# Kernel tuning notes

Measured on AMD Instinct MI355X. Metric: run time of the kernel, lower is better.

Reference implementation:

```python
import jax, jax.numpy as jnp
import numpy as np

B, S, D, H = 2, 2048, 1024, 16
HD = D // H
LOCAL_WINDOW = 32
GLOBAL_TOKENS = 16
BLOCK_SIZE = 64
SPARSITY = 0.75


def _structured_mask(seq_len):
    """local_global | block_sparse pattern, vectorized numpy (deterministic)."""
    i = np.arange(seq_len)[:, None]
    j = np.arange(seq_len)[None, :]
    half = LOCAL_WINDOW // 2
    local = np.abs(i - j) <= half  # mask[i, i-16 : i+17]
    glob = (i < GLOBAL_TOKENS) | (j < GLOBAL_TOKENS)
    stride = max(1, seq_len // 64)
    strided = ((i % stride) == 0) & ((j % stride) == 0)
    lg = local | glob | strided
    # block sparse: random blocks kept with prob 1-SPARSITY, diagonal always kept
    nb = (seq_len + BLOCK_SIZE - 1) // BLOCK_SIZE
    rng = np.random.default_rng(0)
    block_mask = rng.random((nb, nb)) > SPARSITY
    np.fill_diagonal(block_mask, True)
    bs = np.kron(block_mask, np.ones((BLOCK_SIZE, BLOCK_SIZE), dtype=bool))[:seq_len, :seq_len]
    return lg | bs


def setup_inputs() -> dict:
    key = jax.random.key(0)
    ks = jax.random.split(key, 12)
    std = 1.0 / np.sqrt(D)
    inp = {
        'query': jax.random.normal(ks[0], (B, S, D), jnp.float32),
        'key': jax.random.normal(ks[1], (B, S, D), jnp.float32),
        'value': jax.random.normal(ks[2], (B, S, D), jnp.float32),
        'Wq': jax.random.normal(ks[3], (D, D), jnp.float32) * std,
        'bq': jnp.zeros((D,), jnp.float32),
        'Wk': jax.random.normal(ks[4], (D, D), jnp.float32) * std,
        'bk': jnp.zeros((D,), jnp.float32),
        'Wv': jax.random.normal(ks[5], (D, D), jnp.float32) * std,
        'bv': jnp.zeros((D,), jnp.float32),
        'Wo': jax.random.normal(ks[6], (D, D), jnp.float32) * std,
        'bo': jnp.zeros((D,), jnp.float32),
        'sparse_mask': jnp.asarray(_structured_mask(S)),
    }
    return inp


def reference(query, key, value, Wq, bq, Wk, bk, Wv, bv, Wo, bo, sparse_mask):
    scale = HD ** -0.5
    # projections -> [B, H, S, HD]
    q = (query @ Wq + bq).reshape(B, S, H, HD).transpose(0, 2, 1, 3)
    k = (key @ Wk + bk).reshape(B, S, H, HD).transpose(0, 2, 1, 3)
    v = (value @ Wv + bv).reshape(B, S, H, HD).transpose(0, 2, 1, 3)
    # dense scores then structured sparse mask (matches original math)
    scores = jnp.einsum('bhqd,bhkd->bhqk', q, k) * scale
    scores = jnp.where(sparse_mask[None, None], scores, -jnp.inf)
    attn = jax.nn.softmax(scores, axis=-1)  # every row has >=1 active entry (global cols)
    out = jnp.einsum('bhqk,bhkd->bhqd', attn, v)
    out = out.transpose(0, 2, 1, 3).reshape(B, S, D)
    out = out @ Wo + bo
    return out, attn
```

## Files before the change

### kernel.cpp

```cpp
#include <hip/hip_runtime.h>
#include <hip/hip_bf16.h>
#include <hip/hip_fp16.h>

using u16 = unsigned short;
using u32 = unsigned int;
using u64 = unsigned long long;

typedef __attribute__((ext_vector_type(8))) short short8;
typedef __attribute__((ext_vector_type(8))) _Float16 half8;
typedef __attribute__((ext_vector_type(4))) _Float16 half4;
typedef __attribute__((ext_vector_type(4))) float f32x4;
typedef __attribute__((ext_vector_type(2))) u32 u32x2;

#define DEVI static __device__ __forceinline__

DEVI float bfu2f(u16 u) { return __builtin_bit_cast(float, (u32)u << 16); }
DEVI u16 f2bfu(float f) { return __builtin_bit_cast(u16, __float2bfloat16(f)); }
DEVI u16 f2hu(float f) { return __builtin_bit_cast(u16, (_Float16)f); }

DEVI f32x4 mfma_f16_(half8 a, half8 b, f32x4 c) {
  return __builtin_amdgcn_mfma_f32_16x16x32_f16(a, b, c, 0, 0, 0);
}
DEVI f32x4 mfma16_f16_(half4 a, half4 b, f32x4 c) {
  return __builtin_amdgcn_mfma_f32_16x16x16f16(a, b, c, 0, 0, 0);
}

#define GLD_LDS16(src, dst) \
  __builtin_amdgcn_global_load_lds((const __attribute__((address_space(1))) void*)(src), \
                                   (__attribute__((address_space(3))) void*)(dst), 16, 0, 0)

#define BAR() __builtin_amdgcn_s_barrier()
#define VMCNT(n) asm volatile("s_waitcnt vmcnt(" #n ")" ::: "memory")

static constexpr int Bsz = 2, S = 2048, D = 1024, H = 16, HD = 64;
static constexpr int MROWS = Bsz * S;
static constexpr size_t OUT_ELEMS = (size_t)Bsz * S * D;
static constexpr float C_EXP2 = 0.18033688f;
static constexpr size_t OFF_WT  = 0;
static constexpr size_t OFF_Q   = 0x800000;
static constexpr size_t OFF_K   = 0x1000000;
static constexpr size_t OFF_V   = 0x1800000;
static constexpr size_t OFF_VT  = 0x2000000;
static constexpr size_t OFF_O   = 0x2800000;
static constexpr size_t OFF_MB  = 0x3000000;
static constexpr size_t OFF_FLG = 0x3080000;

__global__ __launch_bounds__(256) void detect_dtype(
    const u16* __restrict__ q, int* __restrict__ flag)
{
  __shared__ u32 red[256];
  const int tid = threadIdx.x;
  u32 mx = 0;
  for (int i = tid; i < 32768; i += 256) {
    u32 e = (q[2 * i] >> 7) & 0xFF;
    mx = mx > e ? mx : e;
  }
  red[tid] = mx;
  __syncthreads();
  if (tid == 0) {
    u32 m = 0;
    for (int i = 0; i < 256; ++i) m = m > red[i] ? m : red[i];
    flag[0] = (m >= 0x90) ? 1 : 0;
  }
}

__global__ __launch_bounds__(256) void prep_w(
    const void* __restrict__ Wq, const void* __restrict__ Wk,
    const void* __restrict__ Wv, const void* __restrict__ Wo,
    u16* __restrict__ WT, const int* __restrict__ flag)
{
  __shared__ _Float16 t[64][80];
  const int z = blockIdx.z;
  const void* src = z == 0 ? Wq : z == 1 ? Wk : z == 2 ? Wv : Wo;
  u16* dst = WT + (size_t)z * 1024 * 1024;
  const int bx = blockIdx.x, by = blockIdx.y;
  const int tid = threadIdx.x;
  const int r = tid >> 2, ch = tid & 3;
  const int fl = *flag;
  if (fl) {
    const float* s = (const float*)src + (size_t)(by * 64 + r) * 1024 + bx * 64 + ch * 16;
    #pragma unroll
    for (int v = 0; v < 4; ++v) {
      float4 f = ((const float4*)s)[v];
      t[r][ch * 16 + v * 4 + 0] = (_Float16)f.x;
      t[r][ch * 16 + v * 4 + 1] = (_Float16)f.y;
      t[r][ch * 16 + v * 4 + 2] = (_Float16)f.z;
      t[r][ch * 16 + v * 4 + 3] = (_Float16)f.w;
    }
  } else {
    const u16* s = (const u16*)src + (size_t)(by * 64 + r) * 1024 + bx * 64 + ch * 16;
    uint4 a0 = ((const uint4*)s)[0], a1 = ((const uint4*)s)[1];
    u32 wds[8] = {a0.x, a0.y, a0.z, a0.w, a1.x, a1.y, a1.z, a1.w};
    #pragma unroll
    for (int j = 0; j < 8; ++j) {
      t[r][ch * 16 + 2 * j]     = (_Float16)bfu2f((u16)(wds[j] & 0xFFFF));
      t[r][ch * 16 + 2 * j + 1] = (_Float16)bfu2f((u16)(wds[j] >> 16));
    }
  }
  __syncthreads();
  half8 o0, o1;
  #pragma unroll
  for (int i = 0; i < 8; ++i) { o0[i] = t[ch * 16 + i][r]; o1[i] = t[ch * 16 + 8 + i][r]; }
  u16* d = dst + (size_t)(bx * 64 + r) * 1024 + by * 64 + ch * 16;
  *reinterpret_cast<half8*>(d) = o0;
  *reinterpret_cast<half8*>(d + 8) = o1;
}

__global__ __launch_bounds__(256) void mask_bits_kernel(
    const void* __restrict__ mask, u64* __restrict__ mbits)
{
  const u32 w0 = *(const u32*)mask;
  int mode;
  if (w0 == 0x01010101u) mode = 0;
  else if ((w0 & 0xFFFFu) && (w0 >> 16)) mode = 1;
  else mode = 2;
  const int row = blockIdx.x;
  const int w = threadIdx.x >> 6, l = threadIdx.x & 63;
  for (int i = 0; i < 8; ++i) {
    int jw = w * 8 + i;
    size_t idx = (size_t)row * S + jw * 64 + l;
    bool m;
    if (mode == 0)      m = ((const unsigned char*)mask)[idx] != 0;
    else if (mode == 1) m = ((const u16*)mask)[idx] != 0;
    else                m = ((const u32*)mask)[idx] != 0;
    u64 bal = __ballot(m);
    if (l == 0) mbits[(size_t)row * 32 + jw] = bal;
  }
}

template<int A_DYN, int OUT_DYN>
DEVI void gemm_body(const void* __restrict__ A, const _Float16* __restrict__ Bt,
                    const void* __restrict__ bias, void* __restrict__ C,
                    int fl, int tM, int tN, int N, int K,
                    _Float16* As, _Float16* Bs)
{
  const int tid = threadIdx.x;
  const int w = tid >> 6, l = tid & 63;
  const int wr = w >> 1, wc = w & 1;
  const int lg = l >> 4, lc = l & 15;
  const int rr = l >> 3;
  const int gsw = (l & 7) ^ rr;
  const int rsw = lc & 7;
  const int arow = tid >> 2, ach = tid & 3;

  f32x4 acc[2][4] = {};

  for (int k0 = 0; k0 < K; k0 += 64) {
    if (A_DYN) {
      half8 h0, h1;
      if (fl) {
        const float* ap = (const float*)A + (size_t)(tM + arow) * K + k0 + ach * 16;
        float4 f0 = ((const float4*)ap)[0], f1 = ((const float4*)ap)[1];
        float4 f2 = ((const float4*)ap)[2], f3 = ((const float4*)ap)[3];
        h0[0] = (_Float16)f0.x; h0[1] = (_Float16)f0.y;
        h0[2] = (_Float16)f0.z; h0[3] = (_Float16)f0.w;
        h0[4] = (_Float16)f1.x; h0[5] = (_Float16)f1.y;
        h0[6] = (_Float16)f1.z; h0[7] = (_Float16)f1.w;
        h1[0] = (_Float16)f2.x; h1[1] = (_Float16)f2.y;
        h1[2] = (_Float16)f2.z; h1[3] = (_Float16)f2.w;
        h1[4] = (_Float16)f3.x; h1[5] = (_Float16)f3.y;
        h1[6] = (_Float16)f3.z; h1[7] = (_Float16)f3.w;
      } else {
        const u16* ap = (const u16*)A + (size_t)(tM + arow) * K + k0 + ach * 16;
        uint4 a0 = ((const uint4*)ap)[0], a1 = ((const uint4*)ap)[1];
        u32 wd[8] = {a0.x, a0.y, a0.z, a0.w, a1.x, a1.y, a1.z, a1.w};
        #pragma unroll
        for (int j = 0; j < 4; ++j) {
          h0[2 * j]     = (_Float16)bfu2f((u16)(wd[j] & 0xFFFF));
          h0[2 * j + 1] = (_Float16)bfu2f((u16)(wd[j] >> 16));
          h1[2 * j]     = (_Float16)bfu2f((u16)(wd[4 + j] & 0xFFFF));
          h1[2 * j + 1] = (_Float16)bfu2f((u16)(wd[4 + j] >> 16));
        }
      }
      const int c0 = (2 * ach) ^ (arow & 7), c1 = (2 * ach + 1) ^ (arow & 7);
      *reinterpret_cast<half8*>(&As[arow * 64 + c0 * 8]) = h0;
      *reinterpret_cast<half8*>(&As[arow * 64 + c1 * 8]) = h1;
    } else {
      #pragma unroll
      for (int s = 0; s < 2; ++s)
        GLD_LDS16((const _Float16*)A + (size_t)(tM + w * 16 + s * 8 + rr) * K + k0 + gsw * 8,
                  &As[(w * 16 + s * 8) * 64]);
    }
    #pragma unroll
    for (int s = 0; s < 4; ++s)
      GLD_LDS16(Bt + (size_t)(tN + w * 32 + s * 8 + rr) * K + k0 + gsw * 8,
                &Bs[(w * 32 + s * 8) * 64]);
    __syncthreads();
    half8 a[2][2], b[4][2];
    #pragma unroll
    for (int m = 0; m < 2; ++m)
      #pragma unroll
      for (int kk = 0; kk < 2; ++kk)
        a[m][kk] = *reinterpret_cast<const half8*>(
            &As[(wr * 32 + m * 16 + lc) * 64 + ((kk * 4 + lg) ^ rsw) * 8]);
    #pragma unroll
    for (int n = 0; n < 4; ++n)
      #pragma unroll
      for (int kk = 0; kk < 2; ++kk)
        b[n][kk] = *reinterpret_cast<const half8*>(
            &Bs[(wc * 64 + n * 16 + lc) * 64 + ((kk * 4 + lg) ^ rsw) * 8]);
    #pragma unroll
    for (int m = 0; m < 2; ++m)
      #pragma unroll
      for (int n = 0; n < 4; ++n) {
        acc[m][n] = mfma_f16_(a[m][0], b[n][0], acc[m][n]);
        acc[m][n] = mfma_f16_(a[m][1], b[n][1], acc[m][n]);
      }
    __syncthreads();
  }

  float bf[4];
  #pragma unroll
  for (int n = 0; n < 4; ++n) {
    int col = tN + wc * 64 + n * 16 + lc;
    bf[n] = fl ? ((const float*)bias)[col] : bfu2f(((const u16*)bias)[col]);
  }
  #pragma unroll
  for (int m = 0; m < 2; ++m) {
    int row = tM + wr * 32 + m * 16 + lg * 4;
    #pragma unroll
    for (int n = 0; n < 4; ++n) {
      int col = tN + wc * 64 + n * 16 + lc;
      #pragma unroll
      for (int r = 0; r < 4; ++r) {
        float v = acc[m][n][r] + bf[n];
        size_t off = (size_t)(row + r) * N + col;
        if (OUT_DYN) {
          if (fl) ((float*)C)[off] = v;
          else    ((u16*)C)[off] = f2bfu(v);
        } else {
          ((u16*)C)[off] = f2hu(v);
        }
      }
    }
  }
}

__global__ __launch_bounds__(256) void gemm_qkv(
    const void* __restrict__ Aq, const void* __restrict__ Ak,
    const void* __restrict__ Av, const u16* __restrict__ WT,
    const void* __restrict__ bq, const void* __restrict__ bk,
    const void* __restrict__ bv,
    u16* __restrict__ Qb, u16* __restrict__ Kb, u16* __restrict__ Vb,
    const int* __restrict__ flag)
{
  __shared__ _Float16 As[64 * 64];
  __shared__ _Float16 Bs[128 * 64];
  const int z = blockIdx.z;
  const void* A = z == 0 ? Aq : z == 1 ? Ak : Av;
  const _Float16* Bt = (const _Float16*)(WT + (size_t)z * 1048576);
  const void* bias = z == 0 ? bq : z == 1 ? bk : bv;
  void* C = z == 0 ? Qb : z == 1 ? Kb : Vb;
  gemm_body<1, 0>(A, Bt, bias, C, *flag,
                  blockIdx.x * 64, blockIdx.y * 128, D, D, As, Bs);
}

__global__ __launch_bounds__(256) void gemm_o(
    const _Float16* __restrict__ A, const u16* __restrict__ WoT,
    const void* __restrict__ bias, void* __restrict__ C,
    const int* __restrict__ flag)
{
  __shared__ _Float16 As[64 * 64];
  __shared__ _Float16 Bs[128 * 64];
  gemm_body<0, 1>(A, (const _Float16*)WoT, bias, C, *flag,
                  blockIdx.x * 64, blockIdx.y * 128, D, D, As, Bs);
}

__global__ __launch_bounds__(256) void transpose_v(
    const _Float16* __restrict__ V, _Float16* __restrict__ vT)
{
  __shared__ _Float16 t[64][80];
  const int sb = blockIdx.x, bh = blockIdx.y;
  const int b = bh >> 4, h = bh & 15;
  const int tid = threadIdx.x;
  #pragma unroll
  for (int rep = 0; rep < 2; ++rep) {
    int idx = rep * 256 + tid;
    int sl = idx >> 3, ch = idx & 7;
    *reinterpret_cast<uint4*>(&t[sl][ch * 8]) =
      *reinterpret_cast<const uint4*>(V + (size_t)(b * S + sb * 64 + sl) * D + h * HD + ch * 8);
  }
  __syncthreads();
  #pragma unroll
  for (int rep = 0; rep < 2; ++rep) {
    int idx = rep * 256 + tid;
    int hd = idx >> 3, ch = idx & 7;
    half8 ov;
    #pragma unroll
    for (int i = 0; i < 8; ++i) ov[i] = t[ch * 8 + i][hd];
    *reinterpret_cast<half8*>(vT + ((size_t)bh * HD + hd) * S + sb * 64 + ch * 8) = ov;
  }
}

__global__ __launch_bounds__(256) void attn_kernel(
    const _Float16* __restrict__ Q, const _Float16* __restrict__ Kp,
    const _Float16* __restrict__ vT, const u64* __restrict__ mbits,
    _Float16* __restrict__ O, void* __restrict__ dOut,
    const int* __restrict__ flag)
{
  __shared__ _Float16 Ks[2][4096];
  __shared__ _Float16 Vs[2][4096];

  const int tid = threadIdx.x, w = tid >> 6, l = tid & 63;
  const int lg = l >> 4, lc = l & 15;
  const int flat = blockIdx.y * 32 + blockIdx.x;
  const int nf = (flat & 7) * 128 + (flat >> 3);
  const int rb = nf & 31, bh = nf >> 5;
  const int b = bh >> 4, h = bh & 15;
  const int wg = w ^ (rb & 1);
  const int wrow = rb * 64 + wg * 16;
  const int fl = *flag;

  half8 aq[2];
  {
    const _Float16* qp = Q + (size_t)(b * S + wrow + lc) * D + h * HD;
    aq[0] = *reinterpret_cast<const half8*>(qp + lg * 8);
    aq[1] = *reinterpret_cast<const half8*>(qp + 32 + lg * 8);
  }
  const _Float16* kbase = Kp + (size_t)(b * S) * D + h * HD;
  const _Float16* vbase = vT + (size_t)bh * HD * S;
  const u64* mrow = mbits + (size_t)(wrow + lc) * 32;

  const int rr = w * 8 + (l >> 3);
  const int gsw = (l & 7) ^ (rr & 7);

  #define STAGE_K(buf, jb) do { \
    const _Float16* s0_ = kbase + (size_t)((jb) * 64 + rr) * D + gsw * 8; \
    GLD_LDS16(s0_, &Ks[buf][w * 512]); \
    GLD_LDS16(s0_ + (size_t)32 * D, &Ks[buf][2048 + w * 512]); \
  } while (0)
  #define STAGE_V(buf, jb) do { \
    const _Float16* s0_ = vbase + (size_t)rr * S + (jb) * 64 + gsw * 8; \
    GLD_LDS16(s0_, &Vs[buf][w * 512]); \
    GLD_LDS16(s0_ + (size_t)32 * S, &Vs[buf][2048 + w * 512]); \
  } while (0)

  const int sw = lc & 7;

  float rs = 0.f;
  f32x4 accO[4] = {};

  STAGE_K(0, 0);
  STAGE_V(0, 0);
  u64 mb = mrow[0];

  #pragma unroll 1
  for (int jb = 0; jb < 32; ++jb) {
    const int buf = jb & 1;
    BAR();
    if (jb < 31) {
      STAGE_K(buf ^ 1, jb + 1);
      STAGE_V(buf ^ 1, jb + 1);
      VMCNT(5);
    } else {
      VMCNT(1);
    }
    BAR();
    const u64 mb_next = (jb < 31) ? mrow[jb + 1] : 0ull;
    const _Float16* kt = Ks[buf];
    const _Float16* vt = Vs[buf];
    #pragma unroll
    for (int c = 0; c < 4; ++c) {
      const u32 bits = (u32)(mb >> (c * 16 + lg * 4)) & 0xFu;
      if (__any(bits != 0)) {
        const int r = c * 16 + lc;
        half8 ka = *reinterpret_cast<const half8*>(&kt[r * 64 + ((lg ^ sw) * 8)]);
        half8 kb = *reinterpret_cast<const half8*>(&kt[r * 64 + (((lg + 4) ^ sw) * 8)]);
        f32x4 sc = {};
        sc = mfma_f16_(ka, aq[0], sc);
        sc = mfma_f16_(kb, aq[1], sc);
        half4 pa;
        #pragma unroll
        for (int r2 = 0; r2 < 4; ++r2) {
          float p = ((bits >> r2) & 1) ? exp2f(sc[r2] * C_EXP2) : 0.f;
          rs += p;
          pa[r2] = (_Float16)p;
        }
        #pragma unroll
        for (int d = 0; d < 4; ++d) {
          const int rd = d * 16 + lc;
          const int ch = (2 * c + (lg >> 1)) ^ sw;
          half4 vv = *reinterpret_cast<const half4*>(&vt[rd * 64 + ch * 8 + (lg & 1) * 4]);
          accO[d] = mfma16_f16_(pa, vv, accO[d]);
        }
      }
    }
    mb = mb_next;
  }

  rs += __shfl_xor(rs, 16);
  rs += __shfl_xor(rs, 32);
  const float inv = 1.f / rs;
  const float lg2i = -__log2f(rs);

  float invr[4];
  #pragma unroll
  for (int r = 0; r < 4; ++r) invr[r] = __shfl(inv, lg * 4 + r);

  {
    _Float16* op = O + (size_t)(b * S + wrow + lg * 4) * D + h * HD;
    #pragma unroll
    for (int d = 0; d < 4; ++d)
      #pragma unroll
      for (int r = 0; r < 4; ++r)
        op[(size_t)r * D + d * 16 + lc] = (_Float16)(accO[d][r] * invr[r]);
  }

  STAGE_K(0, 0);
  mb = mrow[0];

  if (fl) {
    float* ar = (float*)dOut + OUT_ELEMS + (size_t)bh * S * S + (size_t)(wrow + lc) * S;
    #pragma unroll 1
    for (int jb = 0; jb < 32; ++jb) {
      const int buf = jb & 1;
      BAR();
      if (jb < 31) { STAGE_K(buf ^ 1, jb + 1); VMCNT(7); }
      else VMCNT(5);
      BAR();
      const u64 mb_next = (jb < 31) ? mrow[jb + 1] : 0ull;
      const _Float16* kt = Ks[buf];
      #pragma unroll
      for (int c = 0; c < 4; ++c) {
        const u32 bits = (u32)(mb >> (c * 16 + lg * 4)) & 0xFu;
        f32x4* dst = (f32x4*)(ar + jb * 64 + c * 16 + lg * 4);
        if (__any(bits != 0)) {
          const int r = c * 16 + lc;
          half8 ka = *reinterpret_cast<const half8*>(&kt[r * 64 + ((lg ^ sw) * 8)]);
          half8 kb = *reinterpret_cast<const half8*>(&kt[r * 64 + (((lg + 4) ^ sw) * 8)]);
          f32x4 sc = {};
          sc = mfma_f16_(ka, aq[0], sc);
          sc = mfma_f16_(kb, aq[1], sc);
          f32x4 pv;
          #pragma unroll
          for (int r2 = 0; r2 < 4; ++r2)
            pv[r2] = ((bits >> r2) & 1) ? exp2f(__builtin_fmaf(sc[r2], C_EXP2, lg2i)) : 0.f;
          *dst = pv;
        } else {
          f32x4 z = {};
          *dst = z;
        }
      }
      mb = mb_next;
    }
  } else {
    u16* ar = (u16*)dOut + OUT_ELEMS + (size_t)bh * S * S + (size_t)(wrow + lc) * S;
    #pragma unroll 1
    for (int jb = 0; jb < 32; ++jb) {
      const int buf = jb & 1;
      BAR();
      if (jb < 31) { STAGE_K(buf ^ 1, jb + 1); VMCNT(7); }
      else VMCNT(5);
      BAR();
      const u64 mb_next = (jb < 31) ? mrow[jb + 1] : 0ull;
      const _Float16* kt = Ks[buf];
      #pragma unroll
      for (int c = 0; c < 4; ++c) {
        const u32 bits = (u32)(mb >> (c * 16 + lg * 4)) & 0xFu;
        u32x2* dst = (u32x2*)(ar + jb * 64 + c * 16 + lg * 4);
        if (__any(bits != 0)) {
          const int r = c * 16 + lc;
          half8 ka = *reinterpret_cast<const half8*>(&kt[r * 64 + ((lg ^ sw) * 8)]);
          half8 kb = *reinterpret_cast<const half8*>(&kt[r * 64 + (((lg + 4) ^ sw) * 8)]);
          f32x4 sc = {};
          sc = mfma_f16_(ka, aq[0], sc);
          sc = mfma_f16_(kb, aq[1], sc);
          float p0 = ((bits >> 0) & 1) ? exp2f(__builtin_fmaf(sc[0], C_EXP2, lg2i)) : 0.f;
          float p1 = ((bits >> 1) & 1) ? exp2f(__builtin_fmaf(sc[1], C_EXP2, lg2i)) : 0.f;
          float p2 = ((bits >> 2) & 1) ? exp2f(__builtin_fmaf(sc[2], C_EXP2, lg2i)) : 0.f;
          float p3 = ((bits >> 3) & 1) ? exp2f(__builtin_fmaf(sc[3], C_EXP2, lg2i)) : 0.f;
          u32x2 pk;
          pk[0] = (u32)f2bfu(p0) | ((u32)f2bfu(p1) << 16);
          pk[1] = (u32)f2bfu(p2) | ((u32)f2bfu(p3) << 16);
          *dst = pk;
        } else {
          u32x2 z = {0, 0};
          *dst = z;
        }
      }
      mb = mb_next;
    }
  }
  #undef STAGE_K
  #undef STAGE_V
}

extern "C" void kernel_launch(void* const* d_in, const int* in_sizes, int n_in,
                              void* d_out, int out_size, void* d_ws, size_t ws_size,
                              hipStream_t stream) {
  const void* query = d_in[0];
  const void* key_  = d_in[1];
  const void* value = d_in[2];
  const void* Wq = d_in[3];  const void* bq = d_in[4];
  const void* Wk = d_in[5];  const void* bk = d_in[6];
  const void* Wv = d_in[7];  const void* bv = d_in[8];
  const void* Wo = d_in[9];  const void* bo = d_in[10];
  const void* mask = d_in[11];

  char* ws = (char*)d_ws;
  u16* WT   = (u16*)(ws + OFF_WT);
  u16* Qb   = (u16*)(ws + OFF_Q);
  u16* Kb   = (u16*)(ws + OFF_K);
  u16* Vb   = (u16*)(ws + OFF_V);
  u16* vTb  = (u16*)(ws + OFF_VT);
  u16* Ob   = (u16*)(ws + OFF_O);
  u64* mbits = (u64*)(ws + OFF_MB);
  int* flag  = (int*)(ws + OFF_FLG);

  u16* WoT = WT + 3145728;

  detect_dtype<<<1, 256, 0, stream>>>((const u16*)query, flag);
  prep_w<<<dim3(16, 16, 4), 256, 0, stream>>>(Wq, Wk, Wv, Wo, WT, flag);
  mask_bits_kernel<<<dim3(S), 256, 0, stream>>>(mask, mbits);

  gemm_qkv<<<dim3(MROWS / 64, D / 128, 3), 256, 0, stream>>>(
      query, key_, value, WT, bq, bk, bv, Qb, Kb, Vb, flag);

  transpose_v<<<dim3(32, 32), 256, 0, stream>>>((const _Float16*)Vb, (_Float16*)vTb);
  attn_kernel<<<dim3(32, 32), 256, 0, stream>>>(
      (const _Float16*)Qb, (const _Float16*)Kb, (const _Float16*)vTb,
      mbits, (_Float16*)Ob, d_out, flag);
  gemm_o<<<dim3(MROWS / 64, D / 128), 256, 0, stream>>>(
      (const _Float16*)Ob, WoT, bo, d_out, flag);
}
```

Before: 326.3 us.

## Split attention into output pass and separate column-halved probability-write kernel

The fused attention kernel is split in two. The first pass computes the output and stores per-row log-sum values to workspace. A second kernel, launched after the output projection, recomputes the scores and writes the dense attention-probability matrix. That second kernel uses twice as many blocks, each covering half the key columns, to spread the large store across more workgroups. The cost is recomputing QK^T and an extra launch, in exchange for more parallelism on the store-bound probability write and shorter per-block work.

```diff
diff --git a/kernel.cpp b/kernel.cpp
--- a/kernel.cpp
+++ b/kernel.cpp
@@ -44,6 +44,7 @@
 static constexpr size_t OFF_O   = 0x2800000;
 static constexpr size_t OFF_MB  = 0x3000000;
 static constexpr size_t OFF_FLG = 0x3080000;
+static constexpr size_t OFF_LGI = 0x3081000;
 
 __global__ __launch_bounds__(256) void detect_dtype(
     const u16* __restrict__ q, int* __restrict__ flag)
@@ -292,11 +293,10 @@
   }
 }
 
-__global__ __launch_bounds__(256) void attn_kernel(
+__global__ __launch_bounds__(256) void attn1_kernel(
     const _Float16* __restrict__ Q, const _Float16* __restrict__ Kp,
     const _Float16* __restrict__ vT, const u64* __restrict__ mbits,
-    _Float16* __restrict__ O, void* __restrict__ dOut,
-    const int* __restrict__ flag)
+    _Float16* __restrict__ O, float* __restrict__ lgi)
 {
   __shared__ _Float16 Ks[2][4096];
   __shared__ _Float16 Vs[2][4096];
@@ -309,7 +309,6 @@
   const int b = bh >> 4, h = bh & 15;
   const int wg = w ^ (rb & 1);
   const int wrow = rb * 64 + wg * 16;
-  const int fl = *flag;
 
   half8 aq[2];
   {
@@ -387,11 +386,12 @@
     }
     mb = mb_next;
   }
+  #undef STAGE_K
+  #undef STAGE_V
 
   rs += __shfl_xor(rs, 16);
   rs += __shfl_xor(rs, 32);
   const float inv = 1.f / rs;
-  const float lg2i = -__log2f(rs);
 
   float invr[4];
   #pragma unroll
@@ -406,19 +406,63 @@
         op[(size_t)r * D + d * 16 + lc] = (_Float16)(accO[d][r] * invr[r]);
   }
 
-  STAGE_K(0, 0);
-  mb = mrow[0];
+  if (l < 16) lgi[(size_t)bh * S + wrow + l] = -__log2f(rs);
+}
+
+__global__ __launch_bounds__(256) void attn2_kernel(
+    const _Float16* __restrict__ Q, const _Float16* __restrict__ Kp,
+    const u64* __restrict__ mbits, const float* __restrict__ lgi,
+    void* __restrict__ dOut, const int* __restrict__ flag)
+{
+  __shared__ _Float16 Ks[2][4096];
+
+  const int tid = threadIdx.x, w = tid >> 6, l = tid & 63;
+  const int lg = l >> 4, lc = l & 15;
+  const int flat = blockIdx.x;
+  const int nf = (flat & 7) * 256 + (flat >> 3);
+  const int bh = nf >> 6;
+  const int rem = nf & 63;
+  const int rb = rem >> 1, half = rem & 1;
+  const int b = bh >> 4, h = bh & 15;
+  const int wg = w ^ (rb & 1);
+  const int wrow = rb * 64 + wg * 16;
+  const int fl = *flag;
+
+  half8 aq[2];
+  {
+    const _Float16* qp = Q + (size_t)(b * S + wrow + lc) * D + h * HD;
+    aq[0] = *reinterpret_cast<const half8*>(qp + lg * 8);
+    aq[1] = *reinterpret_cast<const half8*>(qp + 32 + lg * 8);
+  }
+  const _Float16* kbase = Kp + (size_t)(b * S) * D + h * HD;
+  const u64* mrow = mbits + (size_t)(wrow + lc) * 32;
+  const float lg2i = lgi[(size_t)bh * S + wrow + lc];
+
+  const int rr = w * 8 + (l >> 3);
+  const int gsw = (l & 7) ^ (rr & 7);
+  const int sw = lc & 7;
+  const int jb0 = half * 16;
+
+  #define STAGE_K(buf, jb) do { \
+    const _Float16* s0_ = kbase + (size_t)((jb) * 64 + rr) * D + gsw * 8; \
+    GLD_LDS16(s0_, &Ks[buf][w * 512]); \
+    GLD_LDS16(s0_ + (size_t)32 * D, &Ks[buf][2048 + w * 512]); \
+  } while (0)
+
+  STAGE_K(0, jb0);
+  u64 mb = mrow[jb0];
 
   if (fl) {
     float* ar = (float*)dOut + OUT_ELEMS + (size_t)bh * S * S + (size_t)(wrow + lc) * S;
     #pragma unroll 1
-    for (int jb = 0; jb < 32; ++jb) {
-      const int buf = jb & 1;
+    for (int jj = 0; jj < 16; ++jj) {
+      const int jb = jb0 + jj;
+      const int buf = jj & 1;
       BAR();
-      if (jb < 31) { STAGE_K(buf ^ 1, jb + 1); VMCNT(7); }
+      if (jj < 15) { STAGE_K(buf ^ 1, jb + 1); VMCNT(7); }
       else VMCNT(5);
       BAR();
-      const u64 mb_next = (jb < 31) ? mrow[jb + 1] : 0ull;
+      const u64 mb_next = (jj < 15) ? mrow[jb + 1] : 0ull;
       const _Float16* kt = Ks[buf];
       #pragma unroll
       for (int c = 0; c < 4; ++c) {
@@ -446,13 +490,14 @@
   } else {
     u16* ar = (u16*)dOut + OUT_ELEMS + (size_t)bh * S * S + (size_t)(wrow + lc) * S;
     #pragma unroll 1
-    for (int jb = 0; jb < 32; ++jb) {
-      const int buf = jb & 1;
+    for (int jj = 0; jj < 16; ++jj) {
+      const int jb = jb0 + jj;
+      const int buf = jj & 1;
       BAR();
-      if (jb < 31) { STAGE_K(buf ^ 1, jb + 1); VMCNT(7); }
+      if (jj < 15) { STAGE_K(buf ^ 1, jb + 1); VMCNT(7); }
       else VMCNT(5);
       BAR();
-      const u64 mb_next = (jb < 31) ? mrow[jb + 1] : 0ull;
+      const u64 mb_next = (jj < 15) ? mrow[jb + 1] : 0ull;
       const _Float16* kt = Ks[buf];
       #pragma unroll
       for (int c = 0; c < 4; ++c) {
@@ -482,7 +527,6 @@
     }
   }
   #undef STAGE_K
-  #undef STAGE_V
 }
 
 extern "C" void kernel_launch(void* const* d_in, const int* in_sizes, int n_in,
@@ -506,6 +550,7 @@
   u16* Ob   = (u16*)(ws + OFF_O);
   u64* mbits = (u64*)(ws + OFF_MB);
   int* flag  = (int*)(ws + OFF_FLG);
+  float* lgi = (float*)(ws + OFF_LGI);
 
   u16* WoT = WT + 3145728;
 
@@ -517,9 +562,11 @@
       query, key_, value, WT, bq, bk, bv, Qb, Kb, Vb, flag);
 
   transpose_v<<<dim3(32, 32), 256, 0, stream>>>((const _Float16*)Vb, (_Float16*)vTb);
-  attn_kernel<<<dim3(32, 32), 256, 0, stream>>>(
+  attn1_kernel<<<dim3(32, 32), 256, 0, stream>>>(
       (const _Float16*)Qb, (const _Float16*)Kb, (const _Float16*)vTb,
-      mbits, (_Float16*)Ob, d_out, flag);
+      mbits, (_Float16*)Ob, lgi);
   gemm_o<<<dim3(MROWS / 64, D / 128), 256, 0, stream>>>(
       (const _Float16*)Ob, WoT, bo, d_out, flag);
-}
+  attn2_kernel<<<dim3(2048), 256, 0, stream>>>(
+      (const _Float16*)Qb, (const _Float16*)Kb, mbits, lgi, d_out, flag);
+}
```

Result: slower. 358.2 us (+9.8%).

## Double attention block to 128 query rows with 512 threads sharing K/V tiles

Applied to the files above, without the earlier changes.

The attention kernel now runs 512-thread blocks covering 128 query rows, so each staged 64-key K/V tile in shared memory serves twice as many rows. Each thread issues a single global-to-LDS load per tile instead of two, and the vmcnt waits are retuned to match. The grid halves to 512 blocks, which lowers K/V global traffic but reduces the number of blocks in flight and may lengthen the barrier stalls.

```diff
diff --git a/kernel.cpp b/kernel.cpp
--- a/kernel.cpp
+++ b/kernel.cpp
@@ -292,7 +292,7 @@
   }
 }
 
-__global__ __launch_bounds__(256) void attn_kernel(
+__global__ __launch_bounds__(512) void attn_kernel(
     const _Float16* __restrict__ Q, const _Float16* __restrict__ Kp,
     const _Float16* __restrict__ vT, const u64* __restrict__ mbits,
     _Float16* __restrict__ O, void* __restrict__ dOut,
@@ -303,12 +303,12 @@
 
   const int tid = threadIdx.x, w = tid >> 6, l = tid & 63;
   const int lg = l >> 4, lc = l & 15;
-  const int flat = blockIdx.y * 32 + blockIdx.x;
-  const int nf = (flat & 7) * 128 + (flat >> 3);
-  const int rb = nf & 31, bh = nf >> 5;
+  const int flat = blockIdx.x;
+  const int nf = (flat & 7) * 64 + (flat >> 3);
+  const int bh = nf >> 4, rb2 = nf & 15;
   const int b = bh >> 4, h = bh & 15;
-  const int wg = w ^ (rb & 1);
-  const int wrow = rb * 64 + wg * 16;
+  const int wg = w ^ (rb2 & 1);
+  const int wrow = rb2 * 128 + wg * 16;
   const int fl = *flag;
 
   half8 aq[2];
@@ -321,19 +321,13 @@
   const _Float16* vbase = vT + (size_t)bh * HD * S;
   const u64* mrow = mbits + (size_t)(wrow + lc) * 32;
 
-  const int rr = w * 8 + (l >> 3);
+  const int rr = tid >> 3;
   const int gsw = (l & 7) ^ (rr & 7);
 
-  #define STAGE_K(buf, jb) do { \
-    const _Float16* s0_ = kbase + (size_t)((jb) * 64 + rr) * D + gsw * 8; \
-    GLD_LDS16(s0_, &Ks[buf][w * 512]); \
-    GLD_LDS16(s0_ + (size_t)32 * D, &Ks[buf][2048 + w * 512]); \
-  } while (0)
-  #define STAGE_V(buf, jb) do { \
-    const _Float16* s0_ = vbase + (size_t)rr * S + (jb) * 64 + gsw * 8; \
-    GLD_LDS16(s0_, &Vs[buf][w * 512]); \
-    GLD_LDS16(s0_ + (size_t)32 * S, &Vs[buf][2048 + w * 512]); \
-  } while (0)
+  #define STAGE_K(buf, jb) \
+    GLD_LDS16(kbase + (size_t)((jb) * 64 + rr) * D + gsw * 8, &Ks[buf][w * 512])
+  #define STAGE_V(buf, jb) \
+    GLD_LDS16(vbase + (size_t)rr * S + (jb) * 64 + gsw * 8, &Vs[buf][w * 512])
 
   const int sw = lc & 7;
 
@@ -351,7 +345,7 @@
     if (jb < 31) {
       STAGE_K(buf ^ 1, jb + 1);
       STAGE_V(buf ^ 1, jb + 1);
-      VMCNT(5);
+      VMCNT(3);
     } else {
       VMCNT(1);
     }
@@ -415,8 +409,13 @@
     for (int jb = 0; jb < 32; ++jb) {
       const int buf = jb & 1;
       BAR();
-      if (jb < 31) { STAGE_K(buf ^ 1, jb + 1); VMCNT(7); }
-      else VMCNT(5);
+      if (jb < 31) {
+        STAGE_K(buf ^ 1, jb + 1);
+        if (jb == 0) VMCNT(2);
+        else VMCNT(6);
+      } else {
+        VMCNT(5);
+      }
       BAR();
       const u64 mb_next = (jb < 31) ? mrow[jb + 1] : 0ull;
       const _Float16* kt = Ks[buf];
@@ -449,8 +448,13 @@
     for (int jb = 0; jb < 32; ++jb) {
       const int buf = jb & 1;
       BAR();
-      if (jb < 31) { STAGE_K(buf ^ 1, jb + 1); VMCNT(7); }
-      else VMCNT(5);
+      if (jb < 31) {
+        STAGE_K(buf ^ 1, jb + 1);
+        if (jb == 0) VMCNT(2);
+        else VMCNT(6);
+      } else {
+        VMCNT(5);
+      }
       BAR();
       const u64 mb_next = (jb < 31) ? mrow[jb + 1] : 0ull;
       const _Float16* kt = Ks[buf];
@@ -517,7 +521,7 @@
       query, key_, value, WT, bq, bk, bv, Qb, Kb, Vb, flag);
 
   transpose_v<<<dim3(32, 32), 256, 0, stream>>>((const _Float16*)Vb, (_Float16*)vTb);
-  attn_kernel<<<dim3(32, 32), 256, 0, stream>>>(
+  attn_kernel<<<dim3(512), 512, 0, stream>>>(
       (const _Float16*)Qb, (const _Float16*)Kb, (const _Float16*)vTb,
       mbits, (_Float16*)Ob, d_out, flag);
   gemm_o<<<dim3(MROWS / 64, D / 128), 256, 0, stream>>>(
```

Measured after the change: 315.8 us, median of 2. -3.2%, faster.
